# Performance work log

Measured on AMD Instinct MI355X. Metric: run time of the kernel, lower is better.

The kernel has to match this reference:

```python
import jax, jax.numpy as jnp
import numpy as np

N_NODES = 200_000
N_EDGES = 800_000
IN_DIM = 768
HID = 128
OUT_DIM = 2
NUM_GRAPHS = 1024


def setup_inputs() -> dict:
    key = jax.random.key(0)
    ks = jax.random.split(key, 11)
    x = jax.random.normal(ks[0], (N_NODES, IN_DIM), jnp.float32)
    edge_index = jax.random.randint(ks[1], (2, N_EDGES), 0, N_NODES, dtype=jnp.int32)
    batch = jnp.sort(jax.random.randint(ks[2], (N_NODES,), 0, NUM_GRAPHS, dtype=jnp.int32))

    def lin(kw, kb, fan_in, fan_out):
        bound = 1.0 / np.sqrt(fan_in)
        W = jax.random.uniform(kw, (fan_in, fan_out), jnp.float32, -bound, bound)
        b = jax.random.uniform(kb, (fan_out,), jnp.float32, -bound, bound)
        return W, b

    W_conv, b_conv = lin(ks[3], ks[4], IN_DIM, HID)
    W0, b0 = lin(ks[5], ks[6], IN_DIM, HID)
    W1, b1 = lin(ks[7], ks[8], 2 * HID, HID)
    W2, b2 = lin(ks[9], ks[10], HID, OUT_DIM)
    return {
        "x": x, "edge_index": edge_index, "batch": batch, "num_graphs": NUM_GRAPHS,
        "W_conv": W_conv, "b_conv": b_conv, "W0": W0, "b0": b0,
        "W1": W1, "b1": b1, "W2": W2, "b2": b2,
    }


def gcn_conv(x, edge_index, W, b):
    """PyG GCNConv: add self-loops, D^-1/2 (A+I) D^-1/2 (x W) + b."""
    n = x.shape[0]
    loop = jnp.arange(n, dtype=edge_index.dtype)
    row = jnp.concatenate([edge_index[0], loop])  # source nodes
    col = jnp.concatenate([edge_index[1], loop])  # target nodes
    deg = jax.ops.segment_sum(jnp.ones_like(col, dtype=x.dtype), col, num_segments=n)
    dinv = jnp.where(deg > 0, jax.lax.rsqrt(deg), 0.0)
    norm = dinv[row] * dinv[col]                  # [E+N]
    h = x @ W                                     # [N, HID]
    msg = h[row] * norm[:, None]                  # gather + scale
    out = jax.ops.segment_sum(msg, col, num_segments=n)  # scatter-add
    return out + b


def reference(x, edge_index, batch, num_graphs, W_conv, b_conv, W0, b0, W1, b1, W2, b2):
    out = jax.nn.relu(gcn_conv(x, edge_index, W_conv, b_conv))
    # global_max_pool over sorted batch ids
    pooled = jax.ops.segment_max(out, batch, num_segments=num_graphs)  # [G, HID]
    # first (news/root) node of each graph: batch is sorted, so searchsorted
    # gives the first index where batch == g  (matches nonzero()[0] in torch)
    idx0 = jnp.searchsorted(batch, jnp.arange(num_graphs, dtype=batch.dtype))
    news = jax.nn.relu(x[idx0] @ W0 + b0)                              # [G, HID]
    z = jnp.concatenate([pooled, news], axis=1)                        # [G, 2*HID]
    z = jax.nn.relu(z @ W1 + b1)
    logits = z @ W2 + b2
    return jax.nn.log_softmax(logits, axis=-1)
```

## Files before the change

### kernel.cpp

```cpp
#include <hip/hip_runtime.h>

#define N_NODES 200000
#define N_EDGES 800000
#define IN_DIM 768
#define HID 128
#define NG 1024
#define CAP 32

#define BM 128
#define BKT 32
#define NT (IN_DIM / BKT)
#define GEMM_TILES ((N_NODES + BM - 1) / BM)

#define BIN_BLKS 256
#define BIN_STRIDE (BIN_BLKS * 256)

typedef _Float16 f16x8 __attribute__((ext_vector_type(8)));
typedef float f32x4 __attribute__((ext_vector_type(4)));

__device__ __forceinline__ void gload_lds16(const void* g, void* l) {
  __builtin_amdgcn_global_load_lds((const __attribute__((address_space(1))) void*)g,
                                   (__attribute__((address_space(3))) void*)l, 16, 0, 0);
}

__device__ inline void unpack16(unsigned u, float& a, float& b) {
  union { unsigned v; _Float16 f[2]; } c; c.v = u;
  a = (float)c.f[0]; b = (float)c.f[1];
}
__device__ inline unsigned pack16(float a, float b) {
  union { unsigned v; _Float16 f[2]; } c;
  c.f[0] = (_Float16)a; c.f[1] = (_Float16)b;
  return c.v;
}

__global__ __launch_bounds__(256) void k_prep0(int* __restrict__ cursor,
                                               const float* __restrict__ W, _Float16* __restrict__ WT) {
  int gid = blockIdx.x * 256 + threadIdx.x;
  if (gid < N_NODES) cursor[gid] = 0;
  if (gid < IN_DIM * HID) {
    int k = gid / HID, n = gid % HID;
    WT[(size_t)n * IN_DIM + k] = (_Float16)W[gid];
  }
}

__global__ __launch_bounds__(256, 3) void k_fused(const float* __restrict__ x,
                                                  const _Float16* __restrict__ WT,
                                                  _Float16* __restrict__ h16,
                                                  const int* __restrict__ row, const int* __restrict__ col,
                                                  int* __restrict__ cursor, int* __restrict__ ew) {
  __shared__ __align__(16) char arena[49152];

  if (blockIdx.x >= GEMM_TILES) {
    int gid = ((int)blockIdx.x - GEMM_TILES) * 256 + threadIdx.x;
    for (int e = gid; e < N_EDGES; e += BIN_STRIDE) {
      int c = col[e];
      int slot = atomicAdd(&cursor[c], 1);
      if (slot < CAP) ew[(size_t)c * CAP + slot] = row[e];
    }
    return;
  }

  const int t = threadIdx.x;
  const int lane = t & 63;
  const int wid = t >> 6;
  const int bm = blockIdx.x * BM;

  f32x4 acc[2][8];
#pragma unroll
  for (int i = 0; i < 2; ++i)
#pragma unroll
    for (int j = 0; j < 8; ++j) acc[i][j] = (f32x4){0.f, 0.f, 0.f, 0.f};

  const int lr = lane & 15;
  const int s0 = (lane >> 4) * 2;
  const int bslot_r = lane >> 4;

  const int a_srow = lane >> 3;
  const int a_scol = ((lane & 7) ^ (lane >> 3)) * 4;
  const int b_srow = lane >> 2;
  const int b_scol = (((lane & 3) ^ ((lane >> 3) & 3)) * 8);

  auto stage = [&](int k0, int dbuf) {
    char* bA = arena + dbuf * 16384;
    char* bB = arena + 32768 + dbuf * 8192;
#pragma unroll
    for (int p = 0; p < 4; ++p) {
      int r = p * 32 + wid * 8 + a_srow;
      int grow = bm + r; if (grow >= N_NODES) grow = N_NODES - 1;
      gload_lds16(x + (size_t)grow * IN_DIM + k0 + a_scol, bA + p * 4096 + wid * 1024);
    }
#pragma unroll
    for (int p = 0; p < 2; ++p) {
      int r = p * 64 + wid * 16 + b_srow;
      gload_lds16(WT + (size_t)r * IN_DIM + k0 + b_scol, bB + p * 4096 + wid * 1024);
    }
  };

  stage(0, 0);
  __syncthreads();

  for (int tt = 0; tt < NT; ++tt) {
    const int cur = tt & 1;
    if (tt + 1 < NT) stage((tt + 1) * BKT, cur ^ 1);

    const char* bA = arena + cur * 16384;
    const char* bB = arena + 32768 + cur * 8192;

    f16x8 af[2];
#pragma unroll
    for (int rt = 0; rt < 2; ++rt) {
      int r = wid * 32 + rt * 16 + lr;
      const char* rb = bA + r * 128;
      int f = r & 7;
      float4 lo = *(const float4*)(rb + ((s0 ^ f) << 4));
      float4 hi = *(const float4*)(rb + (((s0 + 1) ^ f) << 4));
      af[rt][0] = (_Float16)lo.x; af[rt][1] = (_Float16)lo.y;
      af[rt][2] = (_Float16)lo.z; af[rt][3] = (_Float16)lo.w;
      af[rt][4] = (_Float16)hi.x; af[rt][5] = (_Float16)hi.y;
      af[rt][6] = (_Float16)hi.z; af[rt][7] = (_Float16)hi.w;
    }
#pragma unroll
    for (int ct = 0; ct < 8; ++ct) {
      int cr = ct * 16 + lr;
      f16x8 bf = *(const f16x8*)(bB + cr * 64 + ((bslot_r ^ ((cr >> 1) & 3)) << 4));
      acc[0][ct] = __builtin_amdgcn_mfma_f32_16x16x32_f16(af[0], bf, acc[0][ct], 0, 0, 0);
      acc[1][ct] = __builtin_amdgcn_mfma_f32_16x16x32_f16(af[1], bf, acc[1][ct], 0, 0, 0);
    }
    __syncthreads();
  }

  _Float16* hb = (_Float16*)arena;
  const int dcol = lane & 15;
  const int drow = (lane >> 4) * 4;
#pragma unroll
  for (int rt = 0; rt < 2; ++rt)
#pragma unroll
    for (int j = 0; j < 4; ++j) {
      int rl = wid * 32 + rt * 16 + drow + j;
#pragma unroll
      for (int ct = 0; ct < 8; ++ct)
        hb[rl * HID + ct * 16 + dcol] = (_Float16)acc[rt][ct][j];
    }
  __syncthreads();
#pragma unroll
  for (int q = 0; q < 8; ++q) {
    int f = t + 256 * q;
    int rowl = f >> 4, seg = f & 15;
    int grow = bm + rowl;
    if (grow < N_NODES)
      ((uint4*)(h16 + (size_t)grow * HID))[seg] = ((const uint4*)hb)[f];
  }
}

__global__ __launch_bounds__(256) void k_gather(const _Float16* __restrict__ h16,
                                                const int* __restrict__ cursor,
                                                const int* __restrict__ ew,
                                                const float* __restrict__ b_conv,
                                                _Float16* __restrict__ hout16) {
  int gid = blockIdx.x * 256 + threadIdx.x;
  int wv = gid >> 6, lane = gid & 63;
  int n0 = wv * 4;
  if (n0 >= N_NODES) return;
  const int grp = lane >> 4;
  const int fl = lane & 15;
  const int j32 = fl + 16 * grp;
  const unsigned* h32 = (const unsigned*)h16;
  unsigned* ho32 = (unsigned*)hout16;
  const float bc0 = b_conv[2 * j32], bc1 = b_conv[2 * j32 + 1];

#pragma unroll
  for (int p = 0; p < 2; ++p) {
    const int iA = n0 + 2 * p;
    const int iB = iA + 1;
    const bool vA = iA < N_NODES, vB = iB < N_NODES;
    const int cA_idx = vA ? iA : N_NODES - 1;
    const int cB_idx = vB ? iB : N_NODES - 1;

    int cntA = cursor[cA_idx];
    int cntB = cursor[cB_idx];
    unsigned selfA = h32[(size_t)cA_idx * 64 + j32];
    unsigned selfB = h32[(size_t)cB_idx * 64 + j32];
    int bkA = (grp < cntA) ? ew[(size_t)cA_idx * CAP + grp] : 0;
    int bkB = (grp < cntB) ? ew[(size_t)cB_idx * CAP + grp] : 0;

    float diA = rsqrtf((float)(cntA + 1));
    float diB = rsqrtf((float)(cntB + 1));
    int mA = cntA > CAP ? CAP : cntA;
    int mB = cntB > CAP ? CAP : cntB;

    float aA[8], aB[8];
#pragma unroll
    for (int q = 0; q < 8; ++q) { aA[q] = 0.f; aB[q] = 0.f; }

    {
      bool eA = grp < (mA < 4 ? mA : 4);
      bool eB = grp < (mB < 4 ? mB : 4);
      float wA = 0.f, wB = 0.f;
      unsigned uA0 = 0, uA1 = 0, uA2 = 0, uA3 = 0;
      unsigned uB0 = 0, uB1 = 0, uB2 = 0, uB3 = 0;
      if (eA) {
        wA = rsqrtf((float)(cursor[bkA] + 1)) * diA;
        const unsigned* hr = h32 + (size_t)bkA * 64;
        uA0 = hr[fl]; uA1 = hr[fl + 16]; uA2 = hr[fl + 32]; uA3 = hr[fl + 48];
      }
      if (eB) {
        wB = rsqrtf((float)(cursor[bkB] + 1)) * diB;
        const unsigned* hr = h32 + (size_t)bkB * 64;
        uB0 = hr[fl]; uB1 = hr[fl + 16]; uB2 = hr[fl + 32]; uB3 = hr[fl + 48];
      }
      float f0, f1;
      unpack16(uA0, f0, f1); aA[0] = fmaf(f0, wA, aA[0]); aA[1] = fmaf(f1, wA, aA[1]);
      unpack16(uA1, f0, f1); aA[2] = fmaf(f0, wA, aA[2]); aA[3] = fmaf(f1, wA, aA[3]);
      unpack16(uA2, f0, f1); aA[4] = fmaf(f0, wA, aA[4]); aA[5] = fmaf(f1, wA, aA[5]);
      unpack16(uA3, f0, f1); aA[6] = fmaf(f0, wA, aA[6]); aA[7] = fmaf(f1, wA, aA[7]);
      unpack16(uB0, f0, f1); aB[0] = fmaf(f0, wB, aB[0]); aB[1] = fmaf(f1, wB, aB[1]);
      unpack16(uB1, f0, f1); aB[2] = fmaf(f0, wB, aB[2]); aB[3] = fmaf(f1, wB, aB[3]);
      unpack16(uB2, f0, f1); aB[4] = fmaf(f0, wB, aB[4]); aB[5] = fmaf(f1, wB, aB[5]);
      unpack16(uB3, f0, f1); aB[6] = fmaf(f0, wB, aB[6]); aB[7] = fmaf(f1, wB, aB[7]);
    }

    int mMax = mA > mB ? mA : mB;
    for (int c = 4; c < mMax; c += 4) {
      bool eA = c + grp < mA;
      bool eB = c + grp < mB;
      int rA = eA ? ew[(size_t)iA * CAP + c + grp] : 0;
      int rB = eB ? ew[(size_t)iB * CAP + c + grp] : 0;
      float wA = 0.f, wB = 0.f;
      unsigned uA0 = 0, uA1 = 0, uA2 = 0, uA3 = 0;
      unsigned uB0 = 0, uB1 = 0, uB2 = 0, uB3 = 0;
      if (eA) {
        wA = rsqrtf((float)(cursor[rA] + 1)) * diA;
        const unsigned* hr = h32 + (size_t)rA * 64;
        uA0 = hr[fl]; uA1 = hr[fl + 16]; uA2 = hr[fl + 32]; uA3 = hr[fl + 48];
      }
      if (eB) {
        wB = rsqrtf((float)(cursor[rB] + 1)) * diB;
        const unsigned* hr = h32 + (size_t)rB * 64;
        uB0 = hr[fl]; uB1 = hr[fl + 16]; uB2 = hr[fl + 32]; uB3 = hr[fl + 48];
      }
      float f0, f1;
      unpack16(uA0, f0, f1); aA[0] = fmaf(f0, wA, aA[0]); aA[1] = fmaf(f1, wA, aA[1]);
      unpack16(uA1, f0, f1); aA[2] = fmaf(f0, wA, aA[2]); aA[3] = fmaf(f1, wA, aA[3]);
      unpack16(uA2, f0, f1); aA[4] = fmaf(f0, wA, aA[4]); aA[5] = fmaf(f1, wA, aA[5]);
      unpack16(uA3, f0, f1); aA[6] = fmaf(f0, wA, aA[6]); aA[7] = fmaf(f1, wA, aA[7]);
      unpack16(uB0, f0, f1); aB[0] = fmaf(f0, wB, aB[0]); aB[1] = fmaf(f1, wB, aB[1]);
      unpack16(uB1, f0, f1); aB[2] = fmaf(f0, wB, aB[2]); aB[3] = fmaf(f1, wB, aB[3]);
      unpack16(uB2, f0, f1); aB[4] = fmaf(f0, wB, aB[4]); aB[5] = fmaf(f1, wB, aB[5]);
      unpack16(uB3, f0, f1); aB[6] = fmaf(f0, wB, aB[6]); aB[7] = fmaf(f1, wB, aB[7]);
    }

#pragma unroll
    for (int q = 0; q < 8; ++q) {
      aA[q] += __shfl_xor(aA[q], 16);
      aA[q] += __shfl_xor(aA[q], 32);
      aB[q] += __shfl_xor(aB[q], 16);
      aB[q] += __shfl_xor(aB[q], 32);
    }
    float rA0 = aA[0], rA1 = aA[1], rB0 = aB[0], rB1 = aB[1];
    if (grp == 1) { rA0 = aA[2]; rA1 = aA[3]; rB0 = aB[2]; rB1 = aB[3]; }
    else if (grp == 2) { rA0 = aA[4]; rA1 = aA[5]; rB0 = aB[4]; rB1 = aB[5]; }
    else if (grp == 3) { rA0 = aA[6]; rA1 = aA[7]; rB0 = aB[6]; rB1 = aB[7]; }

    if (vA) {
      float swA = diA * diA, s0, s1;
      unpack16(selfA, s0, s1);
      float v0 = fmaxf(fmaf(s0, swA, rA0) + bc0, 0.f);
      float v1 = fmaxf(fmaf(s1, swA, rA1) + bc1, 0.f);
      ho32[(size_t)iA * 64 + j32] = pack16(v0, v1);
    }
    if (vB) {
      float swB = diB * diB, s0, s1;
      unpack16(selfB, s0, s1);
      float v0 = fmaxf(fmaf(s0, swB, rB0) + bc0, 0.f);
      float v1 = fmaxf(fmaf(s1, swB, rB1) + bc1, 0.f);
      ho32[(size_t)iB * 64 + j32] = pack16(v0, v1);
    }
  }
}

__global__ __launch_bounds__(128) void k_head(const float* __restrict__ x,
                                              const int* __restrict__ batch,
                                              const _Float16* __restrict__ hout16,
                                              const float* __restrict__ W0, const float* __restrict__ b0,
                                              const float* __restrict__ W1, const float* __restrict__ b1,
                                              const float* __restrict__ W2, const float* __restrict__ b2,
                                              float* __restrict__ out) {
  __shared__ float xr[IN_DIM];
  __shared__ float pl[HID];
  __shared__ float nn[HID];
  __shared__ float red[4];
  int g = blockIdx.x, t = threadIdx.x;

  int lo = 0, hi = N_NODES;
  while (lo < hi) { int mid = (lo + hi) >> 1; if (batch[mid] < g) lo = mid + 1; else hi = mid; }
  int lo2 = 0, hi2 = N_NODES;
  int tgt = g + 1;
  while (lo2 < hi2) { int mid = (lo2 + hi2) >> 1; if (batch[mid] < tgt) lo2 = mid + 1; else hi2 = mid; }
  int i0 = lo < N_NODES ? lo : N_NODES - 1;

  const unsigned* ho32 = (const unsigned*)hout16;
  const int u = t >> 1, half = t & 1;
  float m = 0.f;
  int r = lo;
  for (; r + 3 < lo2; r += 4) {
    unsigned a = ho32[(size_t)r * 64 + u];
    unsigned b = ho32[(size_t)(r + 1) * 64 + u];
    unsigned c = ho32[(size_t)(r + 2) * 64 + u];
    unsigned d = ho32[(size_t)(r + 3) * 64 + u];
    float a0, a1, b0v, b1v, c0, c1, d0, d1;
    unpack16(a, a0, a1); unpack16(b, b0v, b1v);
    unpack16(c, c0, c1); unpack16(d, d0, d1);
    m = fmaxf(m, half ? a1 : a0);
    m = fmaxf(m, half ? b1v : b0v);
    m = fmaxf(m, half ? c1 : c0);
    m = fmaxf(m, half ? d1 : d0);
  }
  for (; r < lo2; ++r) {
    unsigned a = ho32[(size_t)r * 64 + u];
    float a0, a1; unpack16(a, a0, a1);
    m = fmaxf(m, half ? a1 : a0);
  }
  pl[t] = m;

  const float* xp = x + (size_t)i0 * IN_DIM;
  for (int k = t; k < IN_DIM; k += 128) xr[k] = xp[k];
  __syncthreads();

  float a = b0[t];
#pragma unroll 8
  for (int k = 0; k < IN_DIM; ++k) a = fmaf(xr[k], W0[(size_t)k * HID + t], a);
  nn[t] = fmaxf(a, 0.f);
  __syncthreads();

  float z = b1[t];
#pragma unroll 8
  for (int k = 0; k < HID; ++k) z = fmaf(pl[k], W1[(size_t)k * HID + t], z);
#pragma unroll 8
  for (int k = 0; k < HID; ++k) z = fmaf(nn[k], W1[(size_t)(HID + k) * HID + t], z);
  z = fmaxf(z, 0.f);
  float p0 = z * W2[2 * t], p1 = z * W2[2 * t + 1];
#pragma unroll
  for (int o = 32; o > 0; o >>= 1) {
    p0 += __shfl_down(p0, o);
    p1 += __shfl_down(p1, o);
  }
  if ((t & 63) == 0) { red[(t >> 6) * 2] = p0; red[(t >> 6) * 2 + 1] = p1; }
  __syncthreads();
  if (t == 0) {
    float l0 = b2[0] + red[0] + red[2];
    float l1 = b2[1] + red[1] + red[3];
    float mm = fmaxf(l0, l1);
    float lse = mm + logf(expf(l0 - mm) + expf(l1 - mm));
    out[g * 2 + 0] = l0 - lse;
    out[g * 2 + 1] = l1 - lse;
  }
}

extern "C" void kernel_launch(void* const* d_in, const int* in_sizes, int n_in,
                              void* d_out, int out_size, void* d_ws, size_t ws_size,
                              hipStream_t stream) {
  const float* x      = (const float*)d_in[0];
  const int* edge     = (const int*)d_in[1];
  const int* batch    = (const int*)d_in[2];
  const float* W_conv = (const float*)d_in[4];
  const float* b_conv = (const float*)d_in[5];
  const float* W0     = (const float*)d_in[6];
  const float* b0     = (const float*)d_in[7];
  const float* W1     = (const float*)d_in[8];
  const float* b1     = (const float*)d_in[9];
  const float* W2     = (const float*)d_in[10];
  const float* b2     = (const float*)d_in[11];
  float* out = (float*)d_out;

  const int* row = edge;
  const int* col = edge + N_EDGES;

  char* ws = (char*)d_ws;
  _Float16*  h16    = (_Float16*)(ws);
  _Float16*  hout16 = (_Float16*)(ws + 51200000);
  int*       cursor = (int*)  (ws + 102400000);
  int*       ew     = (int*)  (ws + 103200000);
  _Float16*  WT     = (_Float16*)(ws + 128800000);

  k_prep0<<<(N_NODES + 255) / 256, 256, 0, stream>>>(cursor, W_conv, WT);
  k_fused<<<GEMM_TILES + BIN_BLKS, 256, 0, stream>>>(x, WT, h16, row, col, cursor, ew);
  k_gather<<<(((N_NODES + 3) / 4) * 64 + 255) / 256, 256, 0, stream>>>(h16, cursor, ew, b_conv, hout16);
  k_head<<<NG, 128, 0, stream>>>(x, batch, hout16, W0, b0, W1, b1, W2, b2, out);
}
```

Baseline: 328.9 us.

## Double K-tile depth and keep weight fragments in registers loaded from global

Raises the GEMM K-tile from 32 to 64, so half as many barriers run per tile, and switches the A-tile swizzle to a 16-slot XOR pattern over 256-byte rows. The weight (B) operand is no longer staged through LDS. Each wave loads its f16 fragments straight from global/L2 into a double-buffered register array. This frees LDS for a larger A buffer, but raises register pressure and LDS to 64 KB, so launch bounds drop occupancy from 3 to 2 blocks per CU.

Result: slower. 392.5 us (+19.3%).

```diff
diff --git a/kernel.cpp b/kernel.cpp
--- a/kernel.cpp
+++ b/kernel.cpp
@@ -8,7 +8,7 @@
 #define CAP 32
 
 #define BM 128
-#define BKT 32
+#define BKT 64
 #define NT (IN_DIM / BKT)
 #define GEMM_TILES ((N_NODES + BM - 1) / BM)
 
@@ -43,12 +43,12 @@
   }
 }
 
-__global__ __launch_bounds__(256, 3) void k_fused(const float* __restrict__ x,
+__global__ __launch_bounds__(256, 2) void k_fused(const float* __restrict__ x,
                                                   const _Float16* __restrict__ WT,
                                                   _Float16* __restrict__ h16,
                                                   const int* __restrict__ row, const int* __restrict__ col,
                                                   int* __restrict__ cursor, int* __restrict__ ew) {
-  __shared__ __align__(16) char arena[49152];
+  __shared__ __align__(16) char arena[65536];
 
   if (blockIdx.x >= GEMM_TILES) {
     int gid = ((int)blockIdx.x - GEMM_TILES) * 256 + threadIdx.x;
@@ -72,59 +72,64 @@
     for (int j = 0; j < 8; ++j) acc[i][j] = (f32x4){0.f, 0.f, 0.f, 0.f};
 
   const int lr = lane & 15;
-  const int s0 = (lane >> 4) * 2;
-  const int bslot_r = lane >> 4;
-
-  const int a_srow = lane >> 3;
-  const int a_scol = ((lane & 7) ^ (lane >> 3)) * 4;
-  const int b_srow = lane >> 2;
-  const int b_scol = (((lane & 3) ^ ((lane >> 3) & 3)) * 8);
+  const int lk = (lane >> 4) * 8;
 
   auto stage = [&](int k0, int dbuf) {
-    char* bA = arena + dbuf * 16384;
-    char* bB = arena + 32768 + dbuf * 8192;
-#pragma unroll
-    for (int p = 0; p < 4; ++p) {
-      int r = p * 32 + wid * 8 + a_srow;
+    char* bA = arena + dbuf * 32768;
+#pragma unroll
+    for (int p = 0; p < 8; ++p) {
+      int rbase = wid * 32 + p * 4;
+      int r = rbase + (lane >> 4);
       int grow = bm + r; if (grow >= N_NODES) grow = N_NODES - 1;
-      gload_lds16(x + (size_t)grow * IN_DIM + k0 + a_scol, bA + p * 4096 + wid * 1024);
-    }
-#pragma unroll
-    for (int p = 0; p < 2; ++p) {
-      int r = p * 64 + wid * 16 + b_srow;
-      gload_lds16(WT + (size_t)r * IN_DIM + k0 + b_scol, bB + p * 4096 + wid * 1024);
+      int lslot = (lane & 15) ^ (r & 15);
+      gload_lds16(x + (size_t)grow * IN_DIM + k0 + lslot * 4,
+                  bA + rbase * 256);
     }
   };
 
+  f16x8 breg[2][2][8];
+
   stage(0, 0);
-  __syncthreads();
-
+#pragma unroll
+  for (int ks = 0; ks < 2; ++ks)
+#pragma unroll
+    for (int ct = 0; ct < 8; ++ct)
+      breg[0][ks][ct] = *(const f16x8*)(WT + (size_t)(ct * 16 + lr) * IN_DIM + ks * 32 + lk);
+  __syncthreads();
+
+#pragma unroll
   for (int tt = 0; tt < NT; ++tt) {
     const int cur = tt & 1;
-    if (tt + 1 < NT) stage((tt + 1) * BKT, cur ^ 1);
-
-    const char* bA = arena + cur * 16384;
-    const char* bB = arena + 32768 + cur * 8192;
-
-    f16x8 af[2];
-#pragma unroll
-    for (int rt = 0; rt < 2; ++rt) {
-      int r = wid * 32 + rt * 16 + lr;
-      const char* rb = bA + r * 128;
-      int f = r & 7;
-      float4 lo = *(const float4*)(rb + ((s0 ^ f) << 4));
-      float4 hi = *(const float4*)(rb + (((s0 + 1) ^ f) << 4));
-      af[rt][0] = (_Float16)lo.x; af[rt][1] = (_Float16)lo.y;
-      af[rt][2] = (_Float16)lo.z; af[rt][3] = (_Float16)lo.w;
-      af[rt][4] = (_Float16)hi.x; af[rt][5] = (_Float16)hi.y;
-      af[rt][6] = (_Float16)hi.z; af[rt][7] = (_Float16)hi.w;
-    }
-#pragma unroll
-    for (int ct = 0; ct < 8; ++ct) {
-      int cr = ct * 16 + lr;
-      f16x8 bf = *(const f16x8*)(bB + cr * 64 + ((bslot_r ^ ((cr >> 1) & 3)) << 4));
-      acc[0][ct] = __builtin_amdgcn_mfma_f32_16x16x32_f16(af[0], bf, acc[0][ct], 0, 0, 0);
-      acc[1][ct] = __builtin_amdgcn_mfma_f32_16x16x32_f16(af[1], bf, acc[1][ct], 0, 0, 0);
+    if (tt + 1 < NT) {
+      stage((tt + 1) * BKT, cur ^ 1);
+#pragma unroll
+      for (int ks = 0; ks < 2; ++ks)
+#pragma unroll
+        for (int ct = 0; ct < 8; ++ct)
+          breg[cur ^ 1][ks][ct] = *(const f16x8*)(WT + (size_t)(ct * 16 + lr) * IN_DIM
+                                                  + (tt + 1) * BKT + ks * 32 + lk);
+    }
+    const char* bA = arena + cur * 32768;
+#pragma unroll
+    for (int ks = 0; ks < 2; ++ks) {
+      f16x8 af[2];
+#pragma unroll
+      for (int rt = 0; rt < 2; ++rt) {
+        int r = wid * 32 + rt * 16 + lr;
+        const char* rb = bA + r * 256;
+        int s0 = ks * 8 + ((lane >> 4) << 1);
+        float4 lo = *(const float4*)(rb + ((s0 ^ lr) << 4));
+        float4 hi = *(const float4*)(rb + (((s0 + 1) ^ lr) << 4));
+        af[rt][0] = (_Float16)lo.x; af[rt][1] = (_Float16)lo.y;
+        af[rt][2] = (_Float16)lo.z; af[rt][3] = (_Float16)lo.w;
+        af[rt][4] = (_Float16)hi.x; af[rt][5] = (_Float16)hi.y;
+        af[rt][6] = (_Float16)hi.z; af[rt][7] = (_Float16)hi.w;
+      }
+#pragma unroll
+      for (int ct = 0; ct < 8; ++ct) {
+        acc[0][ct] = __builtin_amdgcn_mfma_f32_16x16x32_f16(af[0], breg[cur][ks][ct], acc[0][ct], 0, 0, 0);
+        acc[1][ct] = __builtin_amdgcn_mfma_f32_16x16x32_f16(af[1], breg[cur][ks][ct], acc[1][ct], 0, 0, 0);
+      }
     }
     __syncthreads();
   }
```
